# Performance work log

Hardware: AMD Instinct MI355X
Metric: run time of the kernel (lower is better)

## Reference

```python
import jax, jax.numpy as jnp
import numpy as np

NUM_HEADS = 16
HEAD_DIM = 64
HIDDEN = NUM_HEADS * HEAD_DIM  # 1024


def get_rel_pos(q_size, k_size, rel_pos):
    # q_size == k_size here and rel_pos already has 2*size-1 rows, so the
    # F.interpolate(mode='linear') resize in the original is an identity.
    # relative_coords = q - k + (k_size - 1)  (scale factors are 1.0)
    coords = jnp.arange(q_size)[:, None] - jnp.arange(k_size)[None, :] + (k_size - 1)
    return rel_pos[coords]  # [q_size, k_size, head_dim]


def setup_inputs() -> dict:
    key = jax.random.key(0)
    ks = jax.random.split(key, 7)
    B, H, W = 4, 56, 28
    inp = {
        "hidden_states": jax.random.normal(ks[0], (B, H, W, HIDDEN), jnp.float32),
        "qkv_w": jax.random.normal(ks[1], (3 * HIDDEN, HIDDEN), jnp.float32) * 0.02,
        "qkv_b": jax.random.normal(ks[2], (3 * HIDDEN,), jnp.float32) * 0.02,
        "proj_w": jax.random.normal(ks[3], (HIDDEN, HIDDEN), jnp.float32) * 0.02,
        "proj_b": jax.random.normal(ks[4], (HIDDEN,), jnp.float32) * 0.02,
        "rel_pos_h": jax.random.normal(ks[5], (2 * H - 1, HEAD_DIM), jnp.float32) * 0.02,
        "rel_pos_w": jax.random.normal(ks[6], (2 * W - 1, HEAD_DIM), jnp.float32) * 0.02,
    }
    return inp


def reference(hidden_states, qkv_w, qkv_b, proj_w, proj_b, rel_pos_h, rel_pos_w):
    B, H, W, C = hidden_states.shape
    N = H * W
    scale = HEAD_DIM ** -0.5

    # qkv projection -> [3, B*heads, N, head_dim]
    qkv = hidden_states @ qkv_w.T + qkv_b
    qkv = qkv.reshape(B, N, 3, NUM_HEADS, HEAD_DIM).transpose(2, 0, 3, 1, 4)
    qkv = qkv.reshape(3, B * NUM_HEADS, N, HEAD_DIM)
    query, key_, value = qkv[0], qkv[1], qkv[2]

    # scaled dot-product scores, fully materialized as in the original
    attn = jnp.einsum('bqd,bkd->bqk', query * scale, key_)  # [B*heads, N, N]

    # decomposed relative position bias
    Rh = get_rel_pos(H, H, rel_pos_h)  # [H, H, d]
    Rw = get_rel_pos(W, W, rel_pos_w)  # [W, W, d]
    q_r = query.reshape(B * NUM_HEADS, H, W, HEAD_DIM)
    rel_h = jnp.einsum('bhwc,hkc->bhwk', q_r, Rh)  # [B*heads, H, W, H]
    rel_w = jnp.einsum('bhwc,wkc->bhwk', q_r, Rw)  # [B*heads, H, W, W]
    attn = attn.reshape(B * NUM_HEADS, H, W, H, W)
    attn = attn + rel_h[:, :, :, :, None] + rel_w[:, :, :, None, :]
    attn = attn.reshape(B * NUM_HEADS, N, N)

    attn = jax.nn.softmax(attn.astype(jnp.float32), axis=-1).astype(query.dtype)

    out = jnp.einsum('bqk,bkd->bqd', attn, value)
    out = out.reshape(B, NUM_HEADS, H, W, HEAD_DIM).transpose(0, 2, 3, 1, 4)
    out = out.reshape(B, H, W, C)
    out = out @ proj_w.T + proj_b
    return out
```

## Files before the change

kernel.cpp:

```cpp
#include <hip/hip_runtime.h>
#include <hip/hip_bf16.h>
#include <stdint.h>

typedef __bf16 bf16;
typedef __bf16 bf16x2 __attribute__((ext_vector_type(2)));
typedef __bf16 bf16x4 __attribute__((ext_vector_type(4)));
typedef __bf16 bf16x8 __attribute__((ext_vector_type(8)));
typedef float f32x4 __attribute__((ext_vector_type(4)));

#define AS1 __attribute__((address_space(1)))
#define AS3 __attribute__((address_space(3)))

static __device__ __forceinline__ float b2f(bf16 x) { return (float)x; }

static __device__ __forceinline__ void async_cp16(const bf16* g, bf16* l) {
    __builtin_amdgcn_global_load_lds((const AS1 void*)g, (AS3 void*)l, 16, 0, 0);
}

static __device__ __forceinline__ bf16x4 cvt4(f32x4 v) {
    bf16x4 r;
    r[0] = (bf16)v[0]; r[1] = (bf16)v[1]; r[2] = (bf16)v[2]; r[3] = (bf16)v[3];
    return r;
}

static __device__ __forceinline__ float fast_exp2(float x) {
#if __has_builtin(__builtin_amdgcn_exp2f)
    return __builtin_amdgcn_exp2f(x);
#else
    return __expf(x * 0.69314718056f);
#endif
}

__global__ __launch_bounds__(256) void cvt_kernel(
    const float* __restrict__ src, bf16* __restrict__ dst, int n4) {
    int i = blockIdx.x * 256 + threadIdx.x;
    const int stride = gridDim.x * 256;
    for (; i < n4; i += stride)
        ((bf16x4*)dst)[i] = cvt4(((const f32x4*)src)[i]);
}


#define QKV_EPILOGUE()                                                        \
    for (int nt = 0; nt < 4; nt++) {                                          \
        const int n_ = n0 + wn + nt * 16 + lm;                                \
        const float bv = bias[n_];                                            \
        const int s = n_ >> 10, rem = n_ & 1023;                              \
        const int h = rem >> 6, d = rem & 63;                                 \
        for (int mt = 0; mt < 4; mt++) {                                      \
            for (int r = 0; r < 4; r++) {                                     \
                const int m_ = m0 + wm + mt * 16 + quad * 4 + r;              \
                const int b = m_ / 1568;                                      \
                const int pix = m_ - b * 1568;                                \
                const int g = b * 16 + h;                                     \
                const bf16 v = (bf16)(acc[mt][nt][r] + bv);                   \
                if (s == 0)      Qb[((size_t)g * 1568 + pix) * 64 + d] = v;   \
                else if (s == 1) Kb[((size_t)g * 1568 + pix) * 64 + d] = v;   \
                else {                                                        \
                    const int lk = pix & 31;                                  \
                    const int ppix = (pix & ~31) | ((lk & 15) << 1) | (lk >> 4); \
                    Vt[((size_t)g * 64 + d) * 1568 + ppix] = v;               \
                }                                                             \
            }                                                                 \
        }                                                                     \
    }

__global__ __launch_bounds__(256) void qkv_gemm_bf16(
    const bf16* __restrict__ A, const bf16* __restrict__ W,
    const float* __restrict__ bias, bf16* __restrict__ Qb,
    bf16* __restrict__ Kb, bf16* __restrict__ Vt) {
    __shared__ bf16 As[128 * 32];
    __shared__ bf16 Bs[128 * 32];
    const int t = threadIdx.x;
    const int wid = t >> 6, lane = t & 63;
    const int m0 = blockIdx.x * 128, n0 = blockIdx.y * 128;
    const int wm = (wid & 1) * 64, wn = (wid >> 1) * 64;
    const int r_i = lane >> 2, c8 = (lane & 3) * 8;
    const int lm = lane & 15, quad = lane >> 4;

    f32x4 acc[4][4] = {};
    for (int k0 = 0; k0 < 1024; k0 += 32) {
        __syncthreads();
        for (int i = 0; i < 2; i++) {
            const int blk = wid * 2 + i;
            async_cp16(A + (size_t)(m0 + blk * 16 + r_i) * 1024 + k0 + c8, As + blk * 512);
            async_cp16(W + (size_t)(n0 + blk * 16 + r_i) * 1024 + k0 + c8, Bs + blk * 512);
        }
        __syncthreads();
        bf16x8 af[4], bfr[4];
        for (int x = 0; x < 4; x++) {
            af[x]  = *(const bf16x8*)&As[(wm + x * 16 + lm) * 32 + quad * 8];
            bfr[x] = *(const bf16x8*)&Bs[(wn + x * 16 + lm) * 32 + quad * 8];
        }
        for (int mt = 0; mt < 4; mt++)
            for (int nt = 0; nt < 4; nt++)
                acc[mt][nt] = __builtin_amdgcn_mfma_f32_16x16x32_bf16(af[mt], bfr[nt], acc[mt][nt], 0, 0, 0);
    }
    QKV_EPILOGUE()
}

__global__ __launch_bounds__(256) void qkv_gemm_f32(
    const float* __restrict__ A, const float* __restrict__ W,
    const float* __restrict__ bias, bf16* __restrict__ Qb,
    bf16* __restrict__ Kb, bf16* __restrict__ Vt) {
    __shared__ bf16 As[128 * 32];
    __shared__ bf16 Bs[128 * 32];
    const int t = threadIdx.x;
    const int wid = t >> 6, lane = t & 63;
    const int m0 = blockIdx.x * 128, n0 = blockIdx.y * 128;
    const int wm = (wid & 1) * 64, wn = (wid >> 1) * 64;
    const int lm = lane & 15, quad = lane >> 4;

    f32x4 acc[4][4] = {};
    for (int k0 = 0; k0 < 1024; k0 += 32) {
        __syncthreads();
        for (int i = 0; i < 4; i++) {
            const int idx = t + i * 256;
            const int row = idx >> 3, c4 = (idx & 7) * 4;
            const f32x4 av = *(const f32x4*)&A[(size_t)(m0 + row) * 1024 + k0 + c4];
            const f32x4 wv = *(const f32x4*)&W[(size_t)(n0 + row) * 1024 + k0 + c4];
            *(bf16x4*)&As[row * 32 + c4] = cvt4(av);
            *(bf16x4*)&Bs[row * 32 + c4] = cvt4(wv);
        }
        __syncthreads();
        bf16x8 af[4], bfr[4];
        for (int x = 0; x < 4; x++) {
            af[x]  = *(const bf16x8*)&As[(wm + x * 16 + lm) * 32 + quad * 8];
            bfr[x] = *(const bf16x8*)&Bs[(wn + x * 16 + lm) * 32 + quad * 8];
        }
        for (int mt = 0; mt < 4; mt++)
            for (int nt = 0; nt < 4; nt++)
                acc[mt][nt] = __builtin_amdgcn_mfma_f32_16x16x32_bf16(af[mt], bfr[nt], acc[mt][nt], 0, 0, 0);
    }
    QKV_EPILOGUE()
}

__global__ __launch_bounds__(256) void flash_attn(
    const bf16* __restrict__ Qb, const bf16* __restrict__ Kb,
    const bf16* __restrict__ Vt, const float* __restrict__ rph,
    const float* __restrict__ rpw, bf16* __restrict__ AO) {
    const int x = blockIdx.x;
    const int xcd = x & 7, j = x >> 3;
    const int g = xcd * 8 + j / 25;
    const int qblk = j - (j / 25) * 25;
    const int q0 = qblk * 64;

    __shared__ __align__(16) char smem[38400];
    bf16* Th  = (bf16*)smem;
    bf16* Tw  = (bf16*)(smem + 14592);
    char* B   = smem + 22016;
    bf16* Qs  = (bf16*)B;
    bf16* RPs = (bf16*)B;
    bf16* Ks  = (bf16*)B;
    bf16* Vts = (bf16*)(B + 4608);
    bf16* Ps  = (bf16*)(B + 9728);

    const int t = threadIdx.x, wid = t >> 6, lane = t & 63;
    const int lm = lane & 15, quad = lane >> 4;
    const int qbase_l = wid * 16 + quad * 4;

    for (int c = t; c < 512; c += 256) {
        const int row = c >> 3, col = (c & 7) * 8;
        const int qg = min(q0 + row, 1567);
        *(bf16x8*)&Qs[row * 72 + col] =
            *(const bf16x8*)&Qb[((size_t)g * 1568 + qg) * 64 + col];
    }
    __syncthreads();
    const int qrow_l = wid * 16 + lm;
    const bf16x8 qf0 = *(const bf16x8*)&Qs[qrow_l * 72 + quad * 8];
    const bf16x8 qf1 = *(const bf16x8*)&Qs[qrow_l * 72 + 32 + quad * 8];
    int thb[4], twb[4];
#pragma unroll
    for (int r = 0; r < 4; r++) {
        const int qg = min(q0 + qbase_l + r, 1567);
        const int hq = qg / 28;
        thb[r] = (qbase_l + r) * 114 + hq + 55;
        twb[r] = (qbase_l + r) * 58 + (qg - hq * 28) + 27;
    }
    __syncthreads();

    for (int c = t; c < 1776; c += 256) {
        const int row = c >> 4, col = (c & 15) * 4;
        *(bf16x4*)&RPs[row * 72 + col] = cvt4(*(const f32x4*)&rph[row * 64 + col]);
    }
    __syncthreads();
    f32x4 acch[7];
#pragma unroll
    for (int nt = 0; nt < 7; nt++) {
        const bf16x8 b0 = *(const bf16x8*)&RPs[(nt * 16 + lm) * 72 + quad * 8];
        const bf16x8 b1 = *(const bf16x8*)&RPs[(nt * 16 + lm) * 72 + 32 + quad * 8];
        f32x4 a = {};
        a = __builtin_amdgcn_mfma_f32_16x16x32_bf16(qf0, b0, a, 0, 0, 0);
        a = __builtin_amdgcn_mfma_f32_16x16x32_bf16(qf1, b1, a, 0, 0, 0);
        acch[nt] = a;
    }
    __syncthreads();

    for (int c = t; c < 880; c += 256) {
        const int row = c >> 4, col = (c & 15) * 4;
        *(bf16x4*)&RPs[row * 72 + col] = cvt4(*(const f32x4*)&rpw[row * 64 + col]);
    }
#pragma unroll
    for (int nt = 0; nt < 7; nt++)
#pragma unroll
        for (int r = 0; r < 4; r++)
            Th[(qbase_l + r) * 114 + nt * 16 + lm] = (bf16)(acch[nt][r] * 8.0f);
    __syncthreads();
#pragma unroll
    for (int nt = 0; nt < 4; nt++) {
        const bf16x8 b0 = *(const bf16x8*)&RPs[(nt * 16 + lm) * 72 + quad * 8];
        const bf16x8 b1 = *(const bf16x8*)&RPs[(nt * 16 + lm) * 72 + 32 + quad * 8];
        f32x4 a = {};
        a = __builtin_amdgcn_mfma_f32_16x16x32_bf16(qf0, b0, a, 0, 0, 0);
        a = __builtin_amdgcn_mfma_f32_16x16x32_bf16(qf1, b1, a, 0, 0, 0);
        const int col = nt * 16 + lm;
        if (col < 58) {
#pragma unroll
            for (int r = 0; r < 4; r++)
                Tw[(qbase_l + r) * 58 + col] = (bf16)(a[r] * 8.0f);
        }
    }

    f32x4 o[4] = {};
    float l_lane[4] = {0.f, 0.f, 0.f, 0.f};
    const float C2 = 0.125f * 1.44269504f;
    const float S2 = 10.0f * 1.44269504f;

    const int ks_k = t >> 3, ks_d = (t & 7) * 8;
    const int vs_d = t >> 2, vs_k = (t & 3) * 8;
    bf16* Pw = &Ps[wid * 640];

    int hk0 = 0, wk0 = lm;
    int hk1 = (16 + lm) >= 28 ? 1 : 0;
    int wk1 = 16 + lm - (hk1 ? 28 : 0);

    const size_t kgbase = ((size_t)g * 1568 + ks_k) * 64 + ks_d;
    const size_t vgbase = ((size_t)g * 64 + vs_d) * 1568 + vs_k;
    bf16x8 kreg = *(const bf16x8*)&Kb[kgbase];
    bf16x8 vreg = *(const bf16x8*)&Vt[vgbase];

    for (int kt = 0; kt < 49; kt++) {
        f32x4 s0, s1;
#pragma unroll
        for (int r = 0; r < 4; r++) {
            s0[r] = b2f(Th[thb[r] - hk0]) + b2f(Tw[twb[r] - wk0]);
            s1[r] = b2f(Th[thb[r] - hk1]) + b2f(Tw[twb[r] - wk1]);
        }

        __syncthreads();
        *(bf16x8*)&Ks[ks_k * 72 + ks_d] = kreg;
        *(bf16x8*)&Vts[vs_d * 40 + vs_k] = vreg;
        {
            const int ktn = min(kt + 1, 48);
            kreg = *(const bf16x8*)&Kb[kgbase + (size_t)ktn * 2048];
            vreg = *(const bf16x8*)&Vt[vgbase + ktn * 32];
        }
        __syncthreads();

        {
            const bf16x8 ka0 = *(const bf16x8*)&Ks[lm * 72 + quad * 8];
            const bf16x8 ka1 = *(const bf16x8*)&Ks[lm * 72 + 32 + quad * 8];
            s0 = __builtin_amdgcn_mfma_f32_16x16x32_bf16(qf0, ka0, s0, 0, 0, 0);
            s0 = __builtin_amdgcn_mfma_f32_16x16x32_bf16(qf1, ka1, s0, 0, 0, 0);
            const bf16x8 kb0 = *(const bf16x8*)&Ks[(16 + lm) * 72 + quad * 8];
            const bf16x8 kb1 = *(const bf16x8*)&Ks[(16 + lm) * 72 + 32 + quad * 8];
            s1 = __builtin_amdgcn_mfma_f32_16x16x32_bf16(qf0, kb0, s1, 0, 0, 0);
            s1 = __builtin_amdgcn_mfma_f32_16x16x32_bf16(qf1, kb1, s1, 0, 0, 0);
        }

#pragma unroll
        for (int r = 0; r < 4; r++) {
            const float p0 = fast_exp2(fmaf(s0[r], C2, -S2));
            const float p1 = fast_exp2(fmaf(s1[r], C2, -S2));
            l_lane[r] += p0 + p1;
            bf16x2 pp; pp[0] = (bf16)p0; pp[1] = (bf16)p1;
            *(bf16x2*)&Pw[(quad * 4 + r) * 40 + lm * 2] = pp;
        }
        wk0 += 4; hk0 += 1; if (wk0 >= 28) { wk0 -= 28; hk0 += 1; }
        wk1 += 4; hk1 += 1; if (wk1 >= 28) { wk1 -= 28; hk1 += 1; }

        __asm__ volatile("s_waitcnt lgkmcnt(0)" ::: "memory");
        const bf16x8 pf = *(const bf16x8*)&Pw[lm * 40 + quad * 8];
#pragma unroll
        for (int dt = 0; dt < 4; dt++) {
            const bf16x8 vf = *(const bf16x8*)&Vts[(dt * 16 + lm) * 40 + quad * 8];
            o[dt] = __builtin_amdgcn_mfma_f32_16x16x32_bf16(pf, vf, o[dt], 0, 0, 0);
        }
    }

    const int qrow0 = q0 + qbase_l;
    if (q0 + wid * 16 < 1568) {
        const int bo = g >> 4, h = g & 15;
#pragma unroll
        for (int r = 0; r < 4; r++) {
            float ll = l_lane[r];
            for (int off = 1; off < 16; off <<= 1) ll += __shfl_xor(ll, off, 64);
            const float inv = 1.0f / ll;
            const size_t base = ((size_t)bo * 1568 + qrow0 + r) * 1024 + h * 64;
            for (int dt = 0; dt < 4; dt++)
                AO[base + dt * 16 + lm] = (bf16)(o[dt][r] * inv);
        }
    }
}

__global__ __launch_bounds__(256) void proj_gemm_bf16(
    const bf16* __restrict__ A, const bf16* __restrict__ W,
    const float* __restrict__ bias, float* __restrict__ out) {
    __shared__ bf16 As[128 * 32];
    __shared__ bf16 Bs[128 * 32];
    const int t = threadIdx.x;
    const int wid = t >> 6, lane = t & 63;
    const int m0 = blockIdx.x * 128, n0 = blockIdx.y * 128;
    const int wm = (wid & 1) * 64, wn = (wid >> 1) * 64;
    const int r_i = lane >> 2, c8 = (lane & 3) * 8;
    const int lm = lane & 15, quad = lane >> 4;

    f32x4 acc[4][4] = {};
    for (int k0 = 0; k0 < 1024; k0 += 32) {
        __syncthreads();
        for (int i = 0; i < 2; i++) {
            const int blk = wid * 2 + i;
            async_cp16(A + (size_t)(m0 + blk * 16 + r_i) * 1024 + k0 + c8, As + blk * 512);
            async_cp16(W + (size_t)(n0 + blk * 16 + r_i) * 1024 + k0 + c8, Bs + blk * 512);
        }
        __syncthreads();
        bf16x8 af[4], bfr[4];
        for (int x = 0; x < 4; x++) {
            af[x]  = *(const bf16x8*)&As[(wm + x * 16 + lm) * 32 + quad * 8];
            bfr[x] = *(const bf16x8*)&Bs[(wn + x * 16 + lm) * 32 + quad * 8];
        }
        for (int mt = 0; mt < 4; mt++)
            for (int nt = 0; nt < 4; nt++)
                acc[mt][nt] = __builtin_amdgcn_mfma_f32_16x16x32_bf16(af[mt], bfr[nt], acc[mt][nt], 0, 0, 0);
    }
    for (int nt = 0; nt < 4; nt++) {
        const int n_ = n0 + wn + nt * 16 + lm;
        const float bv = bias[n_];
        for (int mt = 0; mt < 4; mt++)
            for (int r = 0; r < 4; r++) {
                const int m_ = m0 + wm + mt * 16 + quad * 4 + r;
                out[(size_t)m_ * 1024 + n_] = acc[mt][nt][r] + bv;
            }
    }
}

__global__ __launch_bounds__(256) void proj_gemm_f32(
    const bf16* __restrict__ A, const float* __restrict__ W,
    const float* __restrict__ bias, float* __restrict__ out) {
    __shared__ bf16 As[128 * 32];
    __shared__ bf16 Bs[128 * 32];
    const int t = threadIdx.x;
    const int wid = t >> 6, lane = t & 63;
    const int m0 = blockIdx.x * 128, n0 = blockIdx.y * 128;
    const int wm = (wid & 1) * 64, wn = (wid >> 1) * 64;
    const int r_i = lane >> 2, c8 = (lane & 3) * 8;
    const int lm = lane & 15, quad = lane >> 4;

    f32x4 acc[4][4] = {};
    for (int k0 = 0; k0 < 1024; k0 += 32) {
        __syncthreads();
        for (int i = 0; i < 2; i++) {
            const int blk = wid * 2 + i;
            async_cp16(A + (size_t)(m0 + blk * 16 + r_i) * 1024 + k0 + c8, As + blk * 512);
        }
        for (int i = 0; i < 4; i++) {
            const int idx = t + i * 256;
            const int row = idx >> 3, c4 = (idx & 7) * 4;
            const f32x4 wv = *(const f32x4*)&W[(size_t)(n0 + row) * 1024 + k0 + c4];
            *(bf16x4*)&Bs[row * 32 + c4] = cvt4(wv);
        }
        __syncthreads();
        bf16x8 af[4], bfr[4];
        for (int x = 0; x < 4; x++) {
            af[x]  = *(const bf16x8*)&As[(wm + x * 16 + lm) * 32 + quad * 8];
            bfr[x] = *(const bf16x8*)&Bs[(wn + x * 16 + lm) * 32 + quad * 8];
        }
        for (int mt = 0; mt < 4; mt++)
            for (int nt = 0; nt < 4; nt++)
                acc[mt][nt] = __builtin_amdgcn_mfma_f32_16x16x32_bf16(af[mt], bfr[nt], acc[mt][nt], 0, 0, 0);
    }
    for (int nt = 0; nt < 4; nt++) {
        const int n_ = n0 + wn + nt * 16 + lm;
        const float bv = bias[n_];
        for (int mt = 0; mt < 4; mt++)
            for (int r = 0; r < 4; r++) {
                const int m_ = m0 + wm + mt * 16 + quad * 4 + r;
                out[(size_t)m_ * 1024 + n_] = acc[mt][nt][r] + bv;
            }
    }
}

extern "C" void kernel_launch(void* const* d_in, const int* in_sizes, int n_in,
                              void* d_out, int out_size, void* d_ws, size_t ws_size,
                              hipStream_t stream) {
    const float* hs     = (const float*)d_in[0];
    const float* qkv_w  = (const float*)d_in[1];
    const float* qkv_b  = (const float*)d_in[2];
    const float* proj_w = (const float*)d_in[3];
    const float* proj_b = (const float*)d_in[4];
    const float* rph    = (const float*)d_in[5];
    const float* rpw    = (const float*)d_in[6];
    float* out = (float*)d_out;

    const size_t GQ = (size_t)64 * 1568 * 64;
    const size_t N_HS = (size_t)6272 * 1024;
    const size_t N_QW = (size_t)3072 * 1024;
    const size_t N_PW = (size_t)1024 * 1024;
    bf16* Qb = (bf16*)d_ws;
    bf16* Kb = Qb + GQ;
    bf16* Vt = Kb + GQ;
    bf16* AO = Vt + GQ;
    bf16* hs_bf    = AO + GQ;
    bf16* qkvw_bf  = hs_bf + N_HS;
    bf16* projw_bf = qkvw_bf + N_QW;
    const size_t need = (4 * GQ + N_HS + N_QW + N_PW) * sizeof(bf16);

    if (ws_size >= need) {
        cvt_kernel<<<512, 256, 0, stream>>>(hs, hs_bf, (int)(N_HS / 4));
        cvt_kernel<<<512, 256, 0, stream>>>(qkv_w, qkvw_bf, (int)(N_QW / 4));
        cvt_kernel<<<256, 256, 0, stream>>>(proj_w, projw_bf, (int)(N_PW / 4));
        qkv_gemm_bf16<<<dim3(49, 24), 256, 0, stream>>>(hs_bf, qkvw_bf, qkv_b, Qb, Kb, Vt);
        flash_attn<<<1600, 256, 0, stream>>>(Qb, Kb, Vt, rph, rpw, AO);
        proj_gemm_bf16<<<dim3(49, 8), 256, 0, stream>>>(AO, projw_bf, proj_b, out);
    } else {
        qkv_gemm_f32<<<dim3(49, 24), 256, 0, stream>>>(hs, qkv_w, qkv_b, Qb, Kb, Vt);
        flash_attn<<<1600, 256, 0, stream>>>(Qb, Kb, Vt, rph, rpw, AO);
        proj_gemm_f32<<<dim3(49, 8), 256, 0, stream>>>(AO, proj_w, proj_b, out);
    }
}
```

Measured before the change: 348.2 us.

## Software-pipeline PV MFMA with double-buffered V/P tiles and fuse conversion kernels

The attention loop now double-buffers the V tile and the probability tile in shared memory. The P·V MFMA for the previous key tile is deferred into the next iteration, between the two barriers, so it overlaps with the K/V staging instead of waiting on an lgkmcnt drain after the softmax writes. Shared memory per block grows from about 38 KB to 47 KB, which may reduce occupancy. Separately, the three fp32-to-bf16 conversion launches are merged into one kernel writing a contiguous destination, saving two launches.

```diff
diff --git a/kernel.cpp b/kernel.cpp
--- a/kernel.cpp
+++ b/kernel.cpp
@@ -31,12 +31,19 @@
 #endif
 }
 
-__global__ __launch_bounds__(256) void cvt_kernel(
-    const float* __restrict__ src, bf16* __restrict__ dst, int n4) {
+__global__ __launch_bounds__(256) void cvt3_kernel(
+    const float* __restrict__ a, const float* __restrict__ b,
+    const float* __restrict__ c, bf16* __restrict__ dst,
+    int na4, int nb4, int ntot4) {
     int i = blockIdx.x * 256 + threadIdx.x;
     const int stride = gridDim.x * 256;
-    for (; i < n4; i += stride)
-        ((bf16x4*)dst)[i] = cvt4(((const f32x4*)src)[i]);
+    for (; i < ntot4; i += stride) {
+        f32x4 v;
+        if (i < na4)            v = ((const f32x4*)a)[i];
+        else if (i < na4 + nb4) v = ((const f32x4*)b)[i - na4];
+        else                    v = ((const f32x4*)c)[i - na4 - nb4];
+        ((bf16x4*)dst)[i] = cvt4(v);
+    }
 }
 
 
@@ -144,7 +151,7 @@
     const int qblk = j - (j / 25) * 25;
     const int q0 = qblk * 64;
 
-    __shared__ __align__(16) char smem[38400];
+    __shared__ __align__(16) char smem[47104];
     bf16* Th  = (bf16*)smem;
     bf16* Tw  = (bf16*)(smem + 14592);
     char* B   = smem + 22016;
@@ -152,7 +159,7 @@
     bf16* RPs = (bf16*)B;
     bf16* Ks  = (bf16*)B;
     bf16* Vts = (bf16*)(B + 4608);
-    bf16* Ps  = (bf16*)(B + 9728);
+    bf16* Ps  = (bf16*)(B + 14848);
 
     const int t = threadIdx.x, wid = t >> 6, lane = t & 63;
     const int lm = lane & 15, quad = lane >> 4;
@@ -227,7 +234,6 @@
 
     const int ks_k = t >> 3, ks_d = (t & 7) * 8;
     const int vs_d = t >> 2, vs_k = (t & 3) * 8;
-    bf16* Pw = &Ps[wid * 640];
 
     int hk0 = 0, wk0 = lm;
     int hk1 = (16 + lm) >= 28 ? 1 : 0;
@@ -239,20 +245,33 @@
     bf16x8 vreg = *(const bf16x8*)&Vt[vgbase];
 
     for (int kt = 0; kt < 49; kt++) {
+        const int vb = kt & 1;
         f32x4 s0, s1;
 #pragma unroll
         for (int r = 0; r < 4; r++) {
             s0[r] = b2f(Th[thb[r] - hk0]) + b2f(Tw[twb[r] - wk0]);
             s1[r] = b2f(Th[thb[r] - hk1]) + b2f(Tw[twb[r] - wk1]);
         }
+        wk0 += 4; hk0 += 1; if (wk0 >= 28) { wk0 -= 28; hk0 += 1; }
+        wk1 += 4; hk1 += 1; if (wk1 >= 28) { wk1 -= 28; hk1 += 1; }
 
         __syncthreads();
         *(bf16x8*)&Ks[ks_k * 72 + ks_d] = kreg;
-        *(bf16x8*)&Vts[vs_d * 40 + vs_k] = vreg;
+        *(bf16x8*)&Vts[vb * 2560 + vs_d * 40 + vs_k] = vreg;
         {
             const int ktn = min(kt + 1, 48);
             kreg = *(const bf16x8*)&Kb[kgbase + (size_t)ktn * 2048];
             vreg = *(const bf16x8*)&Vt[vgbase + ktn * 32];
+        }
+
+        if (kt) {
+            const int ob = vb ^ 1;
+            const bf16x8 pf = *(const bf16x8*)&Ps[ob * 2560 + wid * 640 + lm * 40 + quad * 8];
+#pragma unroll
+            for (int dt = 0; dt < 4; dt++) {
+                const bf16x8 vf = *(const bf16x8*)&Vts[ob * 2560 + (dt * 16 + lm) * 40 + quad * 8];
+                o[dt] = __builtin_amdgcn_mfma_f32_16x16x32_bf16(pf, vf, o[dt], 0, 0, 0);
+            }
         }
         __syncthreads();
 
@@ -267,6 +286,7 @@
             s1 = __builtin_amdgcn_mfma_f32_16x16x32_bf16(qf1, kb1, s1, 0, 0, 0);
         }
 
+        bf16* Pw = &Ps[vb * 2560 + wid * 640];
 #pragma unroll
         for (int r = 0; r < 4; r++) {
             const float p0 = fast_exp2(fmaf(s0[r], C2, -S2));
@@ -275,11 +295,11 @@
             bf16x2 pp; pp[0] = (bf16)p0; pp[1] = (bf16)p1;
             *(bf16x2*)&Pw[(quad * 4 + r) * 40 + lm * 2] = pp;
         }
-        wk0 += 4; hk0 += 1; if (wk0 >= 28) { wk0 -= 28; hk0 += 1; }
-        wk1 += 4; hk1 += 1; if (wk1 >= 28) { wk1 -= 28; hk1 += 1; }
-
-        __asm__ volatile("s_waitcnt lgkmcnt(0)" ::: "memory");
-        const bf16x8 pf = *(const bf16x8*)&Pw[lm * 40 + quad * 8];
+    }
+
+    __asm__ volatile("s_waitcnt lgkmcnt(0)" ::: "memory");
+    {
+        const bf16x8 pf = *(const bf16x8*)&Ps[wid * 640 + lm * 40 + quad * 8];
 #pragma unroll
         for (int dt = 0; dt < 4; dt++) {
             const bf16x8 vf = *(const bf16x8*)&Vts[(dt * 16 + lm) * 40 + quad * 8];
@@ -415,9 +435,9 @@
     const size_t need = (4 * GQ + N_HS + N_QW + N_PW) * sizeof(bf16);
 
     if (ws_size >= need) {
-        cvt_kernel<<<512, 256, 0, stream>>>(hs, hs_bf, (int)(N_HS / 4));
-        cvt_kernel<<<512, 256, 0, stream>>>(qkv_w, qkvw_bf, (int)(N_QW / 4));
-        cvt_kernel<<<256, 256, 0, stream>>>(proj_w, projw_bf, (int)(N_PW / 4));
+        cvt3_kernel<<<1024, 256, 0, stream>>>(hs, qkv_w, proj_w, hs_bf,
+                                              (int)(N_HS / 4), (int)(N_QW / 4),
+                                              (int)((N_HS + N_QW + N_PW) / 4));
         qkv_gemm_bf16<<<dim3(49, 24), 256, 0, stream>>>(hs_bf, qkvw_bf, qkv_b, Qb, Kb, Vt);
         flash_attn<<<1600, 256, 0, stream>>>(Qb, Kb, Vt, rph, rpw, AO);
         proj_gemm_bf16<<<dim3(49, 8), 256, 0, stream>>>(AO, projw_bf, proj_b, out);
```

Result: slower. 357.8 us (+2.8%).
